# Kernel tuning notes

Measured on AMD Instinct MI355X. Metric: run time of the kernel, lower is better.

Reference implementation:

```python
import jax, jax.numpy as jnp
import numpy as np
from jax import lax

N_INPUT = 1024
N_OUTPUT = 1024
B, T = 8, 64


def setup_inputs() -> dict:
    key = jax.random.key(0)
    k1, k2 = jax.random.split(key)
    X = jax.random.normal(k1, (B, T, N_INPUT), dtype=jnp.float32)
    W_init = jax.random.normal(k2, (B, N_OUTPUT, N_INPUT), dtype=jnp.float32) / np.sqrt(N_INPUT)
    return {"X": X, "W_init": W_init}


def reference(X, W_init):
    lr = 1.0 / X.shape[-1]  # self.lr = 1 / n_input

    def step(W, x_t):
        # pre = bmm(W, x_t[...,None]).squeeze(-1)
        pre = jnp.einsum('boi,bi->bo', W, x_t)
        y_t = jax.nn.sigmoid(pre)
        # Oja plasticity rule: dW_ij = y_i * x_j - y_i^2 * W_ij
        dW = jnp.einsum('bo,bi->boi', y_t, x_t) - (y_t ** 2)[..., None] * W
        W_new = W + lr * dW
        return W_new, y_t

    # scan over time (sequential dependency on W)
    _, m_traj = lax.scan(step, W_init, jnp.swapaxes(X, 0, 1))  # [T, B, n_out]
    return jnp.swapaxes(m_traj, 0, 1)  # [B, T, n_out]
```

## Files before the change

### kernel.cpp

```cpp
#include <hip/hip_runtime.h>
#include <hip/hip_bf16.h>


#define BB 8
#define TT 64
#define NI 1024
#define NO 1024
#define NTOT 1088
#define NTILES 68
#define PADBF 1032

typedef __attribute__((ext_vector_type(8))) short bf16x8;
typedef __attribute__((ext_vector_type(4))) float f32x4;

__device__ __forceinline__ short f2bf(float f) {
    __hip_bfloat16 h = __float2bfloat16(f);
    return __builtin_bit_cast(short, h);
}

__global__ __launch_bounds__(256)
void xcvt_kernel(const float* __restrict__ X, ushort* __restrict__ Xb16)
{
    const int i = blockIdx.x * 256 + threadIdx.x;
    const float4 v = *reinterpret_cast<const float4*>(X + (size_t)i * 4);
    short4 s;
    s.x = f2bf(v.x); s.y = f2bf(v.y); s.z = f2bf(v.z); s.w = f2bf(v.w);
    *reinterpret_cast<short4*>(Xb16 + (size_t)i * 4) = s;
}

__global__ __launch_bounds__(256, 4)
void gemm_kernel(const float* __restrict__ X, const float* __restrict__ W0,
                 const ushort* __restrict__ Xb16, float* __restrict__ G)
{
    __shared__ ushort As[16 * PADBF];

    const int tid  = threadIdx.x;
    const int lane = tid & 63;
    const int wave = tid >> 6;
    const int b  = blockIdx.x & 7;
    const int nt = blockIdx.x >> 3;
    const int n0 = nt * 16;
    const int t0 = wave * 16;

    const int r  = lane & 15;
    const int kb = lane >> 4;

    const float* __restrict__ Abase =
        (n0 < NO) ? (W0 + ((size_t)b * NO + n0) * NI)
                  : (X + ((size_t)b * TT + (n0 - NO)) * NI);

    float4 v[16];
#pragma unroll
    for (int j = 0; j < 16; ++j)
        v[j] = *reinterpret_cast<const float4*>(Abase + (size_t)j * NI + tid * 4);
#pragma unroll
    for (int j = 0; j < 16; ++j) {
        short4 s;
        s.x = f2bf(v[j].x); s.y = f2bf(v[j].y); s.z = f2bf(v[j].z); s.w = f2bf(v[j].w);
        *reinterpret_cast<short4*>(&As[j * PADBF + tid * 4]) = s;
    }
    __syncthreads();

    const ushort* __restrict__ Bbase =
        Xb16 + ((size_t)b * TT + t0 + r) * NI + kb * 8;
    const ushort* __restrict__ Ap = &As[r * PADBF + kb * 8];

    f32x4 acc = {0.f, 0.f, 0.f, 0.f};
#pragma unroll 8
    for (int kk = 0; kk < 32; ++kk) {
        const bf16x8 a  = *reinterpret_cast<const bf16x8*>(Ap + kk * 32);
        const bf16x8 bv = *reinterpret_cast<const bf16x8*>(Bbase + kk * 32);
        acc = __builtin_amdgcn_mfma_f32_16x16x32_bf16(a, bv, acc, 0, 0, 0);
    }

    const int tcol = lane & 15;
    const int mrow = (lane >> 4) * 4;
#pragma unroll
    for (int rr = 0; rr < 4; ++rr)
        G[((size_t)b * NTOT + n0 + mrow + rr) * TT + t0 + tcol] = acc[rr];
}

__global__ __launch_bounds__(256, 8)
void scan_kernel(const float* __restrict__ G, float* __restrict__ out)
{
    __shared__ float Sl[TT][TT];
    __shared__ float ybuf[16][68];

    const int tid  = threadIdx.x;
    const int lane = tid & 63;
    const int wave = tid >> 6;
    const int b  = blockIdx.x & 7;
    const int o0 = (blockIdx.x >> 3) * 16;

    {
        const float4* __restrict__ src =
            reinterpret_cast<const float4*>(G + ((size_t)b * NTOT + NO) * TT);
        float4* dst = reinterpret_cast<float4*>(&Sl[0][0]);
#pragma unroll
        for (int q = 0; q < 4; ++q)
            dst[tid + q * 256] = src[tid + q * 256];
    }

    const int r  = lane & 3;
    const int jb = lane >> 2;
    const int row = o0 + wave * 4 + r;

    const float4 uu = *reinterpret_cast<const float4*>(
        G + ((size_t)b * NTOT + row) * TT + jb * 4);
    float u0 = uu.x, u1 = uu.y, u2 = uu.z, u3 = uu.w;

    __syncthreads();

    const float lr   = 1.0f / 1024.0f;
    const float nL2E = -1.44269504f;
    float y0 = 0.f, y1 = 0.f, y2 = 0.f, y3 = 0.f;

#pragma unroll
    for (int t = 0; t < TT; ++t) {
        const int srcl = (t & 0x3C) | r;
        const float uv = ((t & 3) == 0) ? u0 : ((t & 3) == 1) ? u1
                       : ((t & 3) == 2) ? u2 : u3;
        const float pre = __shfl(uv, srcl, 64);

        const float e = __builtin_amdgcn_exp2f(pre * nL2E);
        const float y = __builtin_amdgcn_rcpf(1.0f + e);

        const bool own = (jb == (t >> 2));
        if ((t & 3) == 0) y0 = own ? y : y0;
        if ((t & 3) == 1) y1 = own ? y : y1;
        if ((t & 3) == 2) y2 = own ? y : y2;
        if ((t & 3) == 3) y3 = own ? y : y3;

        const float c2 = lr * y;
        const float c1 = fmaf(-c2, y, 1.0f);

        const float4 s = *reinterpret_cast<const float4*>(&Sl[t][jb * 4]);
        u0 = fmaf(c1, u0, c2 * s.x);
        u1 = fmaf(c1, u1, c2 * s.y);
        u2 = fmaf(c1, u2, c2 * s.z);
        u3 = fmaf(c1, u3, c2 * s.w);
    }

    {
        float4 yv; yv.x = y0; yv.y = y1; yv.z = y2; yv.w = y3;
        *reinterpret_cast<float4*>(&ybuf[wave * 4 + r][jb * 4]) = yv;
    }
    __syncthreads();

    {
        const int t = tid >> 2;
        const int g = tid & 3;
        float4 ov;
        ov.x = ybuf[g * 4 + 0][t];
        ov.y = ybuf[g * 4 + 1][t];
        ov.z = ybuf[g * 4 + 2][t];
        ov.w = ybuf[g * 4 + 3][t];
        *reinterpret_cast<float4*>(
            &out[(size_t)b * TT * NO + (size_t)t * NO + o0 + g * 4]) = ov;
    }
}

extern "C" void kernel_launch(void* const* d_in, const int* in_sizes, int n_in,
                              void* d_out, int out_size, void* d_ws, size_t ws_size,
                              hipStream_t stream) {
    const float* X  = (const float*)d_in[0];
    const float* W0 = (const float*)d_in[1];
    float* out = (float*)d_out;

    float*  G    = (float*)d_ws;
    ushort* Xb16 = (ushort*)((char*)d_ws + 2228224);

    xcvt_kernel<<<512, 256, 0, stream>>>(X, Xb16);
    gemm_kernel<<<BB * NTILES, 256, 0, stream>>>(X, W0, Xb16, G);
    scan_kernel<<<512, 256, 0, stream>>>(G, out);
}
```

Baseline: 33.52 us.

## Pre-convert W to bf16 and stage GEMM panels via direct global-to-LDS loads

```diff
diff --git a/kernel.cpp b/kernel.cpp
--- a/kernel.cpp
+++ b/kernel.cpp
@@ -8,9 +8,9 @@
 #define NO 1024
 #define NTOT 1088
 #define NTILES 68
-#define PADBF 1032
 
 typedef __attribute__((ext_vector_type(8))) short bf16x8;
+typedef __attribute__((ext_vector_type(8))) short short8v;
 typedef __attribute__((ext_vector_type(4))) float f32x4;
 
 __device__ __forceinline__ short f2bf(float f) {
@@ -19,24 +19,39 @@
 }
 
 __global__ __launch_bounds__(256)
-void xcvt_kernel(const float* __restrict__ X, ushort* __restrict__ Xb16)
+void cvt_kernel(const float* __restrict__ W0, const float* __restrict__ X,
+                ushort* __restrict__ Wb16, ushort* __restrict__ Xb16)
 {
-    const int i = blockIdx.x * 256 + threadIdx.x;
-    const float4 v = *reinterpret_cast<const float4*>(X + (size_t)i * 4);
-    short4 s;
-    s.x = f2bf(v.x); s.y = f2bf(v.y); s.z = f2bf(v.z); s.w = f2bf(v.w);
-    *reinterpret_cast<short4*>(Xb16 + (size_t)i * 4) = s;
+    const int t = blockIdx.x * 256 + threadIdx.x;
+#pragma unroll
+    for (int q = 0; q < 2; ++q) {
+        const size_t base = ((size_t)q * 524288 + t) * 8;
+        const float4 v0 = *reinterpret_cast<const float4*>(W0 + base);
+        const float4 v1 = *reinterpret_cast<const float4*>(W0 + base + 4);
+        short8v s;
+        s[0] = f2bf(v0.x); s[1] = f2bf(v0.y); s[2] = f2bf(v0.z); s[3] = f2bf(v0.w);
+        s[4] = f2bf(v1.x); s[5] = f2bf(v1.y); s[6] = f2bf(v1.z); s[7] = f2bf(v1.w);
+        *reinterpret_cast<short8v*>(Wb16 + base) = s;
+    }
+    if (t < 65536) {
+        const size_t base = (size_t)t * 8;
+        const float4 v0 = *reinterpret_cast<const float4*>(X + base);
+        const float4 v1 = *reinterpret_cast<const float4*>(X + base + 4);
+        short8v s;
+        s[0] = f2bf(v0.x); s[1] = f2bf(v0.y); s[2] = f2bf(v0.z); s[3] = f2bf(v0.w);
+        s[4] = f2bf(v1.x); s[5] = f2bf(v1.y); s[6] = f2bf(v1.z); s[7] = f2bf(v1.w);
+        *reinterpret_cast<short8v*>(Xb16 + base) = s;
+    }
 }
 
 __global__ __launch_bounds__(256, 4)
-void gemm_kernel(const float* __restrict__ X, const float* __restrict__ W0,
-                 const ushort* __restrict__ Xb16, float* __restrict__ G)
+void gemm_kernel(const ushort* __restrict__ Wb16, const ushort* __restrict__ Xb16,
+                 float* __restrict__ G)
 {
-    __shared__ ushort As[16 * PADBF];
-
-    const int tid  = threadIdx.x;
-    const int lane = tid & 63;
-    const int wave = tid >> 6;
+    __shared__ __align__(16) ushort As[16 * 1024];
+
+    const int lane = threadIdx.x & 63;
+    const int wave = threadIdx.x >> 6;
     const int b  = blockIdx.x & 7;
     const int nt = blockIdx.x >> 3;
     const int n0 = nt * 16;
@@ -45,32 +60,40 @@
     const int r  = lane & 15;
     const int kb = lane >> 4;
 
-    const float* __restrict__ Abase =
-        (n0 < NO) ? (W0 + ((size_t)b * NO + n0) * NI)
-                  : (X + ((size_t)b * TT + (n0 - NO)) * NI);
-
-    float4 v[16];
-#pragma unroll
-    for (int j = 0; j < 16; ++j)
-        v[j] = *reinterpret_cast<const float4*>(Abase + (size_t)j * NI + tid * 4);
-#pragma unroll
-    for (int j = 0; j < 16; ++j) {
-        short4 s;
-        s.x = f2bf(v[j].x); s.y = f2bf(v[j].y); s.z = f2bf(v[j].z); s.w = f2bf(v[j].w);
-        *reinterpret_cast<short4*>(&As[j * PADBF + tid * 4]) = s;
+    const char* __restrict__ panel = (const char*)(
+        (n0 < NO) ? (Wb16 + ((size_t)b * NO + n0) * NI)
+                  : (Xb16 + ((size_t)b * TT + (n0 - NO)) * NI));
+
+#pragma unroll
+    for (int ii = 0; ii < 8; ++ii) {
+        const int i   = wave * 8 + ii;
+        const int swz = (i >> 1) & 7;
+        const char* src = panel + i * 1024 + ((lane ^ swz) << 4);
+        char* dst = (char*)As + i * 1024;
+        __builtin_amdgcn_global_load_lds(
+            (const __attribute__((address_space(1))) void*)src,
+            (__attribute__((address_space(3))) void*)dst,
+            16, 0, 0);
     }
     __syncthreads();
+
+    const int lanebyte = (r << 11) | ((kb ^ (r & 3)) << 4);
+    const int rbit = (r >> 2) & 1;
+    const char* ApE = (const char*)As + (lanebyte | (rbit << 6));
+    const char* ApO = (const char*)As + (lanebyte | ((rbit ^ 1) << 6));
 
     const ushort* __restrict__ Bbase =
         Xb16 + ((size_t)b * TT + t0 + r) * NI + kb * 8;
-    const ushort* __restrict__ Ap = &As[r * PADBF + kb * 8];
 
     f32x4 acc = {0.f, 0.f, 0.f, 0.f};
 #pragma unroll 8
-    for (int kk = 0; kk < 32; ++kk) {
-        const bf16x8 a  = *reinterpret_cast<const bf16x8*>(Ap + kk * 32);
-        const bf16x8 bv = *reinterpret_cast<const bf16x8*>(Bbase + kk * 32);
-        acc = __builtin_amdgcn_mfma_f32_16x16x32_bf16(a, bv, acc, 0, 0, 0);
+    for (int kk2 = 0; kk2 < 16; ++kk2) {
+        const bf16x8 ae = *reinterpret_cast<const bf16x8*>(ApE + kk2 * 128);
+        const bf16x8 be = *reinterpret_cast<const bf16x8*>(Bbase + kk2 * 64);
+        acc = __builtin_amdgcn_mfma_f32_16x16x32_bf16(ae, be, acc, 0, 0, 0);
+        const bf16x8 ao = *reinterpret_cast<const bf16x8*>(ApO + kk2 * 128);
+        const bf16x8 bo = *reinterpret_cast<const bf16x8*>(Bbase + kk2 * 64 + 32);
+        acc = __builtin_amdgcn_mfma_f32_16x16x32_bf16(ao, bo, acc, 0, 0, 0);
     }
 
     const int tcol = lane & 15;
@@ -169,8 +192,9 @@
 
     float*  G    = (float*)d_ws;
     ushort* Xb16 = (ushort*)((char*)d_ws + 2228224);
-
-    xcvt_kernel<<<512, 256, 0, stream>>>(X, Xb16);
-    gemm_kernel<<<BB * NTILES, 256, 0, stream>>>(X, W0, Xb16, G);
+    ushort* Wb16 = (ushort*)((char*)d_ws + 3276800);
+
+    cvt_kernel<<<2048, 256, 0, stream>>>(W0, X, Wb16, Xb16);
+    gemm_kernel<<<BB * NTILES, 256, 0, stream>>>(Wb16, Xb16, G);
     scan_kernel<<<512, 256, 0, stream>>>(G, out);
 }
```

After: 36.39 us. +8.5%, slower.

## Process two tiles per GEMM block with double-buffered swizzled LDS and register-held B

Applied to the files above, without the earlier changes.

```diff
diff --git a/kernel.cpp b/kernel.cpp
--- a/kernel.cpp
+++ b/kernel.cpp
@@ -8,7 +8,6 @@
 #define NO 1024
 #define NTOT 1088
 #define NTILES 68
-#define PADBF 1032
 
 typedef __attribute__((ext_vector_type(8))) short bf16x8;
 typedef __attribute__((ext_vector_type(4))) float f32x4;
@@ -28,56 +27,104 @@
     *reinterpret_cast<short4*>(Xb16 + (size_t)i * 4) = s;
 }
 
-__global__ __launch_bounds__(256, 4)
+__global__ __launch_bounds__(256, 1)
 void gemm_kernel(const float* __restrict__ X, const float* __restrict__ W0,
                  const ushort* __restrict__ Xb16, float* __restrict__ G)
 {
-    __shared__ ushort As[16 * PADBF];
+    __shared__ __align__(16) ushort As[2][16 * 1024];
 
     const int tid  = threadIdx.x;
     const int lane = tid & 63;
     const int wave = tid >> 6;
-    const int b  = blockIdx.x & 7;
-    const int nt = blockIdx.x >> 3;
-    const int n0 = nt * 16;
-    const int t0 = wave * 16;
+    const int b    = blockIdx.x & 7;
+    const int slot = blockIdx.x >> 3;
+    const int nt0  = slot * 2;
+    const int t0   = wave * 16;
 
     const int r  = lane & 15;
     const int kb = lane >> 4;
 
-    const float* __restrict__ Abase =
-        (n0 < NO) ? (W0 + ((size_t)b * NO + n0) * NI)
-                  : (X + ((size_t)b * TT + (n0 - NO)) * NI);
+    bf16x8 breg[32];
+    {
+        const ushort* __restrict__ Bbase =
+            Xb16 + ((size_t)b * TT + t0 + r) * NI + kb * 8;
+#pragma unroll
+        for (int kk = 0; kk < 32; ++kk)
+            breg[kk] = *reinterpret_cast<const bf16x8*>(Bbase + kk * 32);
+    }
+
+    const int j  = tid >> 4;
+    const int x  = tid & 15;
+    const int sj = (j & 7) << 4;
+
+    const float* __restrict__ Xb = X + (size_t)b * TT * NI;
+    const float* __restrict__ Wb = W0 + (size_t)b * NO * NI;
+#define SRCROW(nt) ((((nt) * 16) < NO) ? (Wb + ((size_t)((nt) * 16) + j) * NI) \
+                                       : (Xb + ((size_t)((nt) * 16 - NO) + j) * NI))
 
     float4 v[16];
-#pragma unroll
-    for (int j = 0; j < 16; ++j)
-        v[j] = *reinterpret_cast<const float4*>(Abase + (size_t)j * NI + tid * 4);
-#pragma unroll
-    for (int j = 0; j < 16; ++j) {
-        short4 s;
-        s.x = f2bf(v[j].x); s.y = f2bf(v[j].y); s.z = f2bf(v[j].z); s.w = f2bf(v[j].w);
-        *reinterpret_cast<short4*>(&As[j * PADBF + tid * 4]) = s;
+    {
+        const float* sr = SRCROW(nt0) + x * 4;
+#pragma unroll
+        for (int c = 0; c < 16; ++c)
+            v[c] = *reinterpret_cast<const float4*>(sr + c * 64);
+    }
+#pragma unroll
+    for (int c = 0; c < 16; ++c) {
+        short4 s4;
+        s4.x = f2bf(v[c].x); s4.y = f2bf(v[c].y);
+        s4.z = f2bf(v[c].z); s4.w = f2bf(v[c].w);
+        char* dst = (char*)As[0] + j * 2048 + c * 128 + ((x * 8) ^ sj);
+        *reinterpret_cast<short4*>(dst) = s4;
     }
     __syncthreads();
 
-    const ushort* __restrict__ Bbase =
-        Xb16 + ((size_t)b * TT + t0 + r) * NI + kb * 8;
-    const ushort* __restrict__ Ap = &As[r * PADBF + kb * 8];
-
-    f32x4 acc = {0.f, 0.f, 0.f, 0.f};
-#pragma unroll 8
-    for (int kk = 0; kk < 32; ++kk) {
-        const bf16x8 a  = *reinterpret_cast<const bf16x8*>(Ap + kk * 32);
-        const bf16x8 bv = *reinterpret_cast<const bf16x8*>(Bbase + kk * 32);
-        acc = __builtin_amdgcn_mfma_f32_16x16x32_bf16(a, bv, acc, 0, 0, 0);
-    }
+    const int lanebyte = (r << 11) | ((kb ^ (r & 3)) << 4);
+    const int rbit = (r >> 2) & 1;
 
     const int tcol = lane & 15;
     const int mrow = (lane >> 4) * 4;
-#pragma unroll
-    for (int rr = 0; rr < 4; ++rr)
-        G[((size_t)b * NTOT + n0 + mrow + rr) * TT + t0 + tcol] = acc[rr];
+
+#pragma unroll
+    for (int p = 0; p < 2; ++p) {
+        if (p == 0) {
+            const float* sr = SRCROW(nt0 + 1) + x * 4;
+#pragma unroll
+            for (int c = 0; c < 16; ++c)
+                v[c] = *reinterpret_cast<const float4*>(sr + c * 64);
+        }
+
+        const char* base = (const char*)As[p] + lanebyte;
+        const char* ApE = base + (rbit << 6);
+        const char* ApO = base + ((rbit ^ 1) << 6);
+
+        f32x4 acc = {0.f, 0.f, 0.f, 0.f};
+#pragma unroll
+        for (int kk2 = 0; kk2 < 16; ++kk2) {
+            const bf16x8 ae = *reinterpret_cast<const bf16x8*>(ApE + kk2 * 128);
+            acc = __builtin_amdgcn_mfma_f32_16x16x32_bf16(ae, breg[2 * kk2], acc, 0, 0, 0);
+            const bf16x8 ao = *reinterpret_cast<const bf16x8*>(ApO + kk2 * 128);
+            acc = __builtin_amdgcn_mfma_f32_16x16x32_bf16(ao, breg[2 * kk2 + 1], acc, 0, 0, 0);
+        }
+
+        const int n0 = (nt0 + p) * 16;
+#pragma unroll
+        for (int rr = 0; rr < 4; ++rr)
+            G[((size_t)b * NTOT + n0 + mrow + rr) * TT + t0 + tcol] = acc[rr];
+
+        if (p == 0) {
+#pragma unroll
+            for (int c = 0; c < 16; ++c) {
+                short4 s4;
+                s4.x = f2bf(v[c].x); s4.y = f2bf(v[c].y);
+                s4.z = f2bf(v[c].z); s4.w = f2bf(v[c].w);
+                char* dst = (char*)As[1] + j * 2048 + c * 128 + ((x * 8) ^ sj);
+                *reinterpret_cast<short4*>(dst) = s4;
+            }
+            __syncthreads();
+        }
+    }
+#undef SRCROW
 }
 
 __global__ __launch_bounds__(256, 8)
@@ -171,6 +218,6 @@
     ushort* Xb16 = (ushort*)((char*)d_ws + 2228224);
 
     xcvt_kernel<<<512, 256, 0, stream>>>(X, Xb16);
-    gemm_kernel<<<BB * NTILES, 256, 0, stream>>>(X, W0, Xb16, G);
+    gemm_kernel<<<34 * BB, 256, 0, stream>>>(X, W0, Xb16, G);
     scan_kernel<<<512, 256, 0, stream>>>(G, out);
 }
```

Measured after the change: 30.19 us. 9.9% less time.

## Split GEMM over K into four partial sums reduced inside the scan kernel

Applied to the files above, without the earlier changes.

```diff
diff --git a/kernel.cpp b/kernel.cpp
--- a/kernel.cpp
+++ b/kernel.cpp
@@ -7,8 +7,7 @@
 #define NI 1024
 #define NO 1024
 #define NTOT 1088
-#define NTILES 68
-#define PADBF 1032
+#define PSTR ((size_t)BB * NTOT * TT)
 
 typedef __attribute__((ext_vector_type(8))) short bf16x8;
 typedef __attribute__((ext_vector_type(4))) float f32x4;
@@ -29,59 +28,72 @@
 }
 
 __global__ __launch_bounds__(256, 4)
-void gemm_kernel(const float* __restrict__ X, const float* __restrict__ W0,
-                 const ushort* __restrict__ Xb16, float* __restrict__ G)
+void gemmp_kernel(const float* __restrict__ X, const float* __restrict__ W0,
+                  const ushort* __restrict__ Xb16, float* __restrict__ Gp)
 {
-    __shared__ ushort As[16 * PADBF];
+    __shared__ __align__(16) ushort As[16 * 264];
 
     const int tid  = threadIdx.x;
     const int lane = tid & 63;
     const int wave = tid >> 6;
-    const int b  = blockIdx.x & 7;
-    const int nt = blockIdx.x >> 3;
-    const int n0 = nt * 16;
-    const int t0 = wave * 16;
+    const int ks  = blockIdx.x & 3;
+    const int job = blockIdx.x >> 2;
+    const int b   = job & 7;
+    const int nt  = job >> 3;
+    const int n0  = nt * 16;
+    const int t0  = wave * 16;
 
     const int r  = lane & 15;
     const int kb = lane >> 4;
 
+    bf16x8 breg[8];
+    {
+        const ushort* __restrict__ Bbase =
+            Xb16 + ((size_t)b * TT + t0 + r) * NI + ks * 256 + kb * 8;
+#pragma unroll
+        for (int kk = 0; kk < 8; ++kk)
+            breg[kk] = *reinterpret_cast<const bf16x8*>(Bbase + kk * 32);
+    }
+
     const float* __restrict__ Abase =
-        (n0 < NO) ? (W0 + ((size_t)b * NO + n0) * NI)
-                  : (X + ((size_t)b * TT + (n0 - NO)) * NI);
-
-    float4 v[16];
-#pragma unroll
-    for (int j = 0; j < 16; ++j)
-        v[j] = *reinterpret_cast<const float4*>(Abase + (size_t)j * NI + tid * 4);
-#pragma unroll
-    for (int j = 0; j < 16; ++j) {
-        short4 s;
-        s.x = f2bf(v[j].x); s.y = f2bf(v[j].y); s.z = f2bf(v[j].z); s.w = f2bf(v[j].w);
-        *reinterpret_cast<short4*>(&As[j * PADBF + tid * 4]) = s;
+        (((n0) < NO) ? (W0 + ((size_t)b * NO + n0) * NI)
+                     : (X + ((size_t)b * TT + (n0 - NO)) * NI)) + ks * 256;
+    {
+        const int j = tid >> 4;
+        const int x = tid & 15;
+        const float* sr = Abase + (size_t)j * NI + x * 16;
+        const float4 v0 = *reinterpret_cast<const float4*>(sr);
+        const float4 v1 = *reinterpret_cast<const float4*>(sr + 4);
+        const float4 v2 = *reinterpret_cast<const float4*>(sr + 8);
+        const float4 v3 = *reinterpret_cast<const float4*>(sr + 12);
+        bf16x8 s0, s1;
+        s0[0] = f2bf(v0.x); s0[1] = f2bf(v0.y); s0[2] = f2bf(v0.z); s0[3] = f2bf(v0.w);
+        s0[4] = f2bf(v1.x); s0[5] = f2bf(v1.y); s0[6] = f2bf(v1.z); s0[7] = f2bf(v1.w);
+        s1[0] = f2bf(v2.x); s1[1] = f2bf(v2.y); s1[2] = f2bf(v2.z); s1[3] = f2bf(v2.w);
+        s1[4] = f2bf(v3.x); s1[5] = f2bf(v3.y); s1[6] = f2bf(v3.z); s1[7] = f2bf(v3.w);
+        *reinterpret_cast<bf16x8*>(&As[j * 264 + x * 16])     = s0;
+        *reinterpret_cast<bf16x8*>(&As[j * 264 + x * 16 + 8]) = s1;
     }
     __syncthreads();
 
-    const ushort* __restrict__ Bbase =
-        Xb16 + ((size_t)b * TT + t0 + r) * NI + kb * 8;
-    const ushort* __restrict__ Ap = &As[r * PADBF + kb * 8];
-
     f32x4 acc = {0.f, 0.f, 0.f, 0.f};
-#pragma unroll 8
-    for (int kk = 0; kk < 32; ++kk) {
-        const bf16x8 a  = *reinterpret_cast<const bf16x8*>(Ap + kk * 32);
-        const bf16x8 bv = *reinterpret_cast<const bf16x8*>(Bbase + kk * 32);
-        acc = __builtin_amdgcn_mfma_f32_16x16x32_bf16(a, bv, acc, 0, 0, 0);
+    const ushort* __restrict__ Ap = &As[r * 264 + kb * 8];
+#pragma unroll
+    for (int kk = 0; kk < 8; ++kk) {
+        const bf16x8 a = *reinterpret_cast<const bf16x8*>(Ap + kk * 32);
+        acc = __builtin_amdgcn_mfma_f32_16x16x32_bf16(a, breg[kk], acc, 0, 0, 0);
     }
 
     const int tcol = lane & 15;
     const int mrow = (lane >> 4) * 4;
+    float* __restrict__ Gout = Gp + (size_t)ks * PSTR;
 #pragma unroll
     for (int rr = 0; rr < 4; ++rr)
-        G[((size_t)b * NTOT + n0 + mrow + rr) * TT + t0 + tcol] = acc[rr];
+        Gout[((size_t)b * NTOT + n0 + mrow + rr) * TT + t0 + tcol] = acc[rr];
 }
 
 __global__ __launch_bounds__(256, 8)
-void scan_kernel(const float* __restrict__ G, float* __restrict__ out)
+void scan_kernel(const float* __restrict__ Gp, float* __restrict__ out)
 {
     __shared__ float Sl[TT][TT];
     __shared__ float ybuf[16][68];
@@ -93,21 +105,41 @@
     const int o0 = (blockIdx.x >> 3) * 16;
 
     {
-        const float4* __restrict__ src =
-            reinterpret_cast<const float4*>(G + ((size_t)b * NTOT + NO) * TT);
+        const size_t off = ((size_t)b * NTOT + NO) * TT;
+        const float4* p0 = reinterpret_cast<const float4*>(Gp + 0 * PSTR + off);
+        const float4* p1 = reinterpret_cast<const float4*>(Gp + 1 * PSTR + off);
+        const float4* p2 = reinterpret_cast<const float4*>(Gp + 2 * PSTR + off);
+        const float4* p3 = reinterpret_cast<const float4*>(Gp + 3 * PSTR + off);
         float4* dst = reinterpret_cast<float4*>(&Sl[0][0]);
 #pragma unroll
-        for (int q = 0; q < 4; ++q)
-            dst[tid + q * 256] = src[tid + q * 256];
+        for (int q = 0; q < 4; ++q) {
+            const int idx = tid + q * 256;
+            const float4 a = p0[idx], c = p1[idx], d = p2[idx], e = p3[idx];
+            float4 s;
+            s.x = a.x + c.x + d.x + e.x;
+            s.y = a.y + c.y + d.y + e.y;
+            s.z = a.z + c.z + d.z + e.z;
+            s.w = a.w + c.w + d.w + e.w;
+            dst[idx] = s;
+        }
     }
 
     const int r  = lane & 3;
     const int jb = lane >> 2;
     const int row = o0 + wave * 4 + r;
 
-    const float4 uu = *reinterpret_cast<const float4*>(
-        G + ((size_t)b * NTOT + row) * TT + jb * 4);
-    float u0 = uu.x, u1 = uu.y, u2 = uu.z, u3 = uu.w;
+    float u0, u1, u2, u3;
+    {
+        const size_t go = ((size_t)b * NTOT + row) * TT + jb * 4;
+        const float4 a = *reinterpret_cast<const float4*>(Gp + 0 * PSTR + go);
+        const float4 c = *reinterpret_cast<const float4*>(Gp + 1 * PSTR + go);
+        const float4 d = *reinterpret_cast<const float4*>(Gp + 2 * PSTR + go);
+        const float4 e = *reinterpret_cast<const float4*>(Gp + 3 * PSTR + go);
+        u0 = a.x + c.x + d.x + e.x;
+        u1 = a.y + c.y + d.y + e.y;
+        u2 = a.z + c.z + d.z + e.z;
+        u3 = a.w + c.w + d.w + e.w;
+    }
 
     __syncthreads();
 
@@ -167,10 +199,10 @@
     const float* W0 = (const float*)d_in[1];
     float* out = (float*)d_out;
 
-    float*  G    = (float*)d_ws;
-    ushort* Xb16 = (ushort*)((char*)d_ws + 2228224);
+    float*  Gp   = (float*)d_ws;
+    ushort* Xb16 = (ushort*)((char*)d_ws + 8912896);
 
     xcvt_kernel<<<512, 256, 0, stream>>>(X, Xb16);
-    gemm_kernel<<<BB * NTILES, 256, 0, stream>>>(X, W0, Xb16, G);
-    scan_kernel<<<512, 256, 0, stream>>>(G, out);
-}
+    gemmp_kernel<<<4 * 544, 256, 0, stream>>>(X, W0, Xb16, Gp);
+    scan_kernel<<<512, 256, 0, stream>>>(Gp, out);
+}
```

New measurement: 31.39 us. 6.4% less time.
